# Kernel optimization log

Hardware: AMD Instinct MI355X
Metric: run time of the kernel (lower is better)

Reference implementation:

```python
import jax, jax.numpy as jnp
import numpy as np

# Module hyperparameters (init_kwargs)
TOP_K = 0.15          # fraction of pixels kept per row when step_percent=1
IGNORE_INDEX = 255

B, K, N, H, W = 8, 3, 8, 384, 384


def setup_inputs() -> dict:
    key = jax.random.key(0)
    k1, k2 = jax.random.split(key)
    # log-probabilities over K classes (nll_loss expects log-probs)
    logits = jax.random.normal(k1, (B, K, N, H, W), dtype=jnp.float32)
    inp = jax.nn.log_softmax(logits, axis=1)
    target = jax.random.randint(k2, (B, N, H, W), 0, K, dtype=jnp.int32)
    return {"input": inp, "target": target, "step_percent": 1}


def reference(input, target, step_percent):
    b, k, n, h, w = input.shape
    P = h * w
    x = input.reshape(b * n, k, P)           # (BN, K, P)
    t = target.reshape(b * n, P)             # (BN, P)

    # per-pixel NLL with ignore_index (ignored pixels contribute 0)
    mask = t != IGNORE_INDEX
    t_safe = jnp.where(mask, t, 0)
    nll = -jnp.take_along_axis(x, t_safe[:, None, :], axis=1)[:, 0, :]  # (BN, P)
    nll = jnp.where(mask, nll, jnp.zeros((), nll.dtype))

    # static k: step_percent is a Python scalar in the original forward
    sp = min(float(step_percent), 1.0)
    n_top_k = int(sp * TOP_K * P + (1.0 - sp) * P)

    top_k_loss, _ = jax.lax.top_k(nll, n_top_k)  # (BN, n_top_k)
    return jnp.mean(top_k_loss)
```

## Files before the change

kernel.cpp:

```cpp
#include <hip/hip_runtime.h>

#define BN    64
#define KCLS  3
#define PPIX  147456
#define NB1   4096
#define NB3   128
#define BPR   36
#define PX_BLK 4096
#define F4_BLK 1024
#define CAP   8192

static const size_t OFF_NLL  = 0;
static const size_t OFF_CAND = OFF_NLL + (size_t)BN * PPIX * 4;
static const size_t OFF_C1   = OFF_CAND + (size_t)BN * CAP * 4;
static const size_t OFF_CCNT = OFF_C1 + (size_t)BN * NB1 * 4;
static const size_t OFF_SS   = OFF_CCNT + 256;
static const size_t OFF_ACC  = OFF_SS + 512;
static const size_t ZERO_END = OFF_ACC + 8;

__device__ __forceinline__ unsigned topk_count(const int* sp_ptr) {
    double sp = (double)sp_ptr[0];
    if (sp > 1.0) sp = 1.0;
    return (unsigned)(sp * 0.15 * (double)PPIX + (1.0 - sp) * (double)PPIX);
}

__device__ __forceinline__ float sel_nll(int t, float a, float b, float c) {
    float lp = (t == 0) ? a : ((t == 1) ? b : ((t == 2) ? c : 0.0f));
    return fmaxf(-lp, 0.0f);
}

__global__ __launch_bounds__(256) void k_hist1(
    const float* __restrict__ in, const int* __restrict__ tgt,
    float* __restrict__ nll, unsigned* __restrict__ cnt1)
{
    __shared__ unsigned lc[NB1];
    const int tid = threadIdx.x;
    for (int i = tid; i < NB1; i += 256) lc[i] = 0u;
    __syncthreads();

    const int row   = blockIdx.x / BPR;
    const int chunk = blockIdx.x % BPR;
    const float4* p0 = (const float4*)(in + (size_t)row * KCLS * PPIX);
    const float4* p1 = p0 + PPIX / 4;
    const float4* p2 = p1 + PPIX / 4;
    const int4*   t4 = (const int4*)(tgt + (size_t)row * PPIX);
    float4*       n4 = (float4*)(nll + (size_t)row * PPIX);
    const int base = chunk * F4_BLK;

    #pragma unroll
    for (int j = 0; j < 4; ++j) {
        const int idx = base + j * 256 + tid;
        const int4   t = t4[idx];
        const float4 a = p0[idx];
        const float4 b = p1[idx];
        const float4 c = p2[idx];
        float4 v;
        v.x = sel_nll(t.x, a.x, b.x, c.x);
        v.y = sel_nll(t.y, a.y, b.y, c.y);
        v.z = sel_nll(t.z, a.z, b.z, c.z);
        v.w = sel_nll(t.w, a.w, b.w, c.w);
        n4[idx] = v;
        atomicAdd(&lc[__float_as_uint(v.x) >> 19], 1u);
        atomicAdd(&lc[__float_as_uint(v.y) >> 19], 1u);
        atomicAdd(&lc[__float_as_uint(v.z) >> 19], 1u);
        atomicAdd(&lc[__float_as_uint(v.w) >> 19], 1u);
    }
    __syncthreads();

    unsigned* gc = cnt1 + (size_t)row * NB1;
    for (int i = tid; i < NB1; i += 256) {
        const unsigned cc = lc[i];
        if (cc) atomicAdd(&gc[i], cc);
    }
}

__global__ __launch_bounds__(256) void k_scan(
    const unsigned* __restrict__ cnt, const int* __restrict__ sp_ptr,
    int* __restrict__ st_b, int* __restrict__ st_r)
{
    const int row = blockIdx.x, tid = threadIdx.x;
    __shared__ unsigned csum[256];
    const unsigned* c = cnt + (size_t)row * NB1;

    unsigned cl[16]; unsigned cacc = 0;
    const int base = tid * 16;
    #pragma unroll
    for (int i = 0; i < 16; ++i) {
        cl[i] = c[NB1 - 1 - (base + i)];
        cacc += cl[i];
    }
    csum[tid] = cacc;
    __syncthreads();
    for (int off = 1; off < 256; off <<= 1) {
        unsigned t2 = (tid >= off) ? csum[tid - off] : 0u;
        __syncthreads();
        csum[tid] += t2;
        __syncthreads();
    }
    const unsigned k = topk_count(sp_ptr);
    unsigned cum = tid ? csum[tid - 1] : 0u;
    #pragma unroll
    for (int i = 0; i < 16; ++i) {
        const unsigned cb = cl[i];
        if (cum < k && cum + cb >= k) {
            st_b[row] = NB1 - 1 - (base + i);
            st_r[row] = (int)(k - cum);
        }
        cum += cb;
    }
}

__global__ __launch_bounds__(256) void k_compact(
    const float* __restrict__ nll, const int* __restrict__ st_b1,
    float* __restrict__ cand, int* __restrict__ ccnt, double* __restrict__ st_S)
{
    __shared__ float  stage[PX_BLK];
    __shared__ double dred[256];
    __shared__ int lcnt, gbase;
    const int tid = threadIdx.x;
    if (tid == 0) lcnt = 0;
    __syncthreads();

    const int row   = blockIdx.x / BPR;
    const int chunk = blockIdx.x % BPR;
    const unsigned b1 = (unsigned)st_b1[row];
    const unsigned lo = b1 << 19;
    const unsigned hi = (b1 + 1u) << 19;
    const float4* n4 = (const float4*)(nll + (size_t)row * PPIX);
    const int base = chunk * F4_BLK;

    double acc = 0.0;
    #pragma unroll
    for (int j = 0; j < 4; ++j) {
        const float4 f = n4[base + j * 256 + tid];
        const float vv[4] = {f.x, f.y, f.z, f.w};
        #pragma unroll
        for (int q = 0; q < 4; ++q) {
            const unsigned u = __float_as_uint(vv[q]);
            if (u >= hi) {
                acc += (double)vv[q];
            } else if (u >= lo) {
                const int s = atomicAdd(&lcnt, 1);
                stage[s] = vv[q];
            }
        }
    }
    dred[tid] = acc;
    __syncthreads();
    for (int s = 128; s > 0; s >>= 1) {
        if (tid < s) dred[tid] += dred[tid + s];
        __syncthreads();
    }
    if (tid == 0) {
        atomicAdd(&st_S[row], dred[0]);
        gbase = atomicAdd(&ccnt[row], lcnt);
    }
    __syncthreads();
    const int n = lcnt, gb = gbase;
    float* cr = cand + (size_t)row * CAP;
    for (int i = tid; i < n; i += 256) {
        const int pos = gb + i;
        if (pos < CAP) cr[pos] = stage[i];
    }
}

__global__ __launch_bounds__(256) void k_resolve(
    const float* __restrict__ cand, const int* __restrict__ ccnt,
    const int* __restrict__ st_b1, const int* __restrict__ st_r1,
    const double* __restrict__ st_S, double* __restrict__ accum)
{
    __shared__ unsigned lc[NB1];
    __shared__ float    ls[NB1];
    __shared__ unsigned csum[256];
    __shared__ double   ssum[256];
    __shared__ int sb2, sr2;
    __shared__ double sS2;

    const int row = blockIdx.x, tid = threadIdx.x;
    int n = ccnt[row]; if (n > CAP) n = CAP;
    const float* cv = cand + (size_t)row * CAP;

    for (int i = tid; i < NB1; i += 256) { lc[i] = 0u; ls[i] = 0.0f; }
    __syncthreads();
    for (int i = tid; i < n; i += 256) {
        const float v = cv[i];
        const unsigned key = (__float_as_uint(v) >> 7) & 0xFFFu;
        atomicAdd(&lc[key], 1u);
        atomicAdd(&ls[key], v);
    }
    __syncthreads();

    unsigned cl[16]; float slv[16];
    unsigned cacc = 0; double sacc = 0.0;
    const int base = tid * 16;
    #pragma unroll
    for (int i = 0; i < 16; ++i) {
        const int bin = NB1 - 1 - (base + i);
        cl[i]  = lc[bin];
        slv[i] = ls[bin];
        cacc += cl[i];
        sacc += (double)slv[i];
    }
    csum[tid] = cacc; ssum[tid] = sacc;
    __syncthreads();
    for (int off = 1; off < 256; off <<= 1) {
        unsigned cv2 = 0; double sv = 0.0;
        if (tid >= off) { cv2 = csum[tid - off]; sv = ssum[tid - off]; }
        __syncthreads();
        csum[tid] += cv2; ssum[tid] += sv;
        __syncthreads();
    }
    const unsigned k = (unsigned)st_r1[row];
    unsigned cum = tid ? csum[tid - 1] : 0u;
    double   sS  = tid ? ssum[tid - 1] : 0.0;
    #pragma unroll
    for (int i = 0; i < 16; ++i) {
        const unsigned cb = cl[i];
        if (cum < k && cum + cb >= k) {
            sb2 = NB1 - 1 - (base + i);
            sr2 = (int)(k - cum);
            sS2 = sS;
        }
        cum += cb;
        sS  += (double)slv[i];
    }
    __syncthreads();

    const unsigned pref = ((unsigned)st_b1[row] << 12) | (unsigned)sb2;
    if (tid < NB3) { lc[tid] = 0u; ls[tid] = 0.0f; }
    __syncthreads();
    for (int i = tid; i < n; i += 256) {
        const float v = cv[i];
        const unsigned bits = __float_as_uint(v);
        if ((bits >> 7) == pref) {
            atomicAdd(&lc[bits & 0x7Fu], 1u);
            atomicAdd(&ls[bits & 0x7Fu], v);
        }
    }
    __syncthreads();
    if (tid == 0) {
        const unsigned k3 = (unsigned)sr2;
        unsigned cum3 = 0, r3 = 0; int b3 = 0; double S3 = 0.0;
        for (int bin = NB3 - 1; bin >= 0; --bin) {
            const unsigned cb = lc[bin];
            if (cum3 < k3 && cum3 + cb >= k3) { b3 = bin; r3 = k3 - cum3; break; }
            cum3 += cb;
            S3   += (double)ls[bin];
        }
        const float tval = __uint_as_float((pref << 7) | (unsigned)b3);
        const double total = st_S[row] + sS2 + S3 + (double)r3 * (double)tval;
        atomicAdd(accum, total);
    }
}

__global__ void k_out(const double* __restrict__ accum, const int* __restrict__ sp_ptr,
                      float* __restrict__ out)
{
    if (threadIdx.x == 0 && blockIdx.x == 0) {
        const unsigned k = topk_count(sp_ptr);
        out[0] = (float)(accum[0] / ((double)BN * (double)k));
    }
}

extern "C" void kernel_launch(void* const* d_in, const int* in_sizes, int n_in,
                              void* d_out, int out_size, void* d_ws, size_t ws_size,
                              hipStream_t stream)
{
    const float* in  = (const float*)d_in[0];
    const int*   tgt = (const int*)d_in[1];
    const int*   sp  = (const int*)d_in[2];

    char* ws = (char*)d_ws;
    float*    nll   = (float*)(ws + OFF_NLL);
    float*    cand  = (float*)(ws + OFF_CAND);
    unsigned* cnt1  = (unsigned*)(ws + OFF_C1);
    int*      ccnt  = (int*)(ws + OFF_CCNT);
    double*   st_S  = (double*)(ws + OFF_SS);
    double*   accum = (double*)(ws + OFF_ACC);
    int*      st_b1 = (int*)(ws + OFF_CCNT + 64 * 4);
    st_b1 = (int*)(ws + ZERO_END);
    int*  st_r1 = (int*)(ws + ZERO_END + 256);

    hipMemsetAsync(ws + OFF_C1, 0, ZERO_END - OFF_C1, stream);

    const int blocks = BN * BPR;
    k_hist1  <<<blocks, 256, 0, stream>>>(in, tgt, nll, cnt1);
    k_scan   <<<BN, 256, 0, stream>>>(cnt1, sp, st_b1, st_r1);
    k_compact<<<blocks, 256, 0, stream>>>(nll, st_b1, cand, ccnt, st_S);
    k_resolve<<<BN, 256, 0, stream>>>(cand, ccnt, st_b1, st_r1, st_S, accum);
    k_out    <<<1, 64, 0, stream>>>(accum, sp, (float*)d_out);
}
```

Baseline: 253.2 us.

## Fuse top-k radix-select pipeline into one cooperative kernel with register-resident NLL

Replaces the five-kernel histogram/scan/compact/resolve/output chain with a single cooperative kernel of 1024 blocks that uses grid-wide syncs between phases. Each thread keeps its per-pixel NLL values in registers across the first grid sync, so the full NLL buffer is never written to or read back from global memory. The scan is recomputed redundantly in every block and the final division happens through a ticket counter. This removes launch gaps and a large global round trip, at the cost of grid-sync overhead and a co-residency requirement of four blocks per CU. If the cooperative launch fails, it falls back to the old multi-kernel path.

```diff
diff --git a/kernel.cpp b/kernel.cpp
--- a/kernel.cpp
+++ b/kernel.cpp
@@ -1,14 +1,24 @@
 #include <hip/hip_runtime.h>
+#include <hip/hip_cooperative_groups.h>
+
+namespace cg = cooperative_groups;
 
 #define BN    64
 #define KCLS  3
 #define PPIX  147456
 #define NB1   4096
 #define NB3   128
-#define BPR   36
+#define CAP   8192
+
+#define NBLK      1024
+#define CPR       16
+#define F4PB      2304
+#define VPT       9
+#define STAGE_CAP 2048
+
+#define BPR    36
+#define F4_BLK 1024
 #define PX_BLK 4096
-#define F4_BLK 1024
-#define CAP   8192
 
 static const size_t OFF_NLL  = 0;
 static const size_t OFF_CAND = OFF_NLL + (size_t)BN * PPIX * 4;
@@ -16,7 +26,10 @@
 static const size_t OFF_CCNT = OFF_C1 + (size_t)BN * NB1 * 4;
 static const size_t OFF_SS   = OFF_CCNT + 256;
 static const size_t OFF_ACC  = OFF_SS + 512;
-static const size_t ZERO_END = OFF_ACC + 8;
+static const size_t OFF_DONE = OFF_ACC + 8;
+static const size_t ZERO_END = OFF_DONE + 8;
+static const size_t OFF_B1   = ZERO_END;
+static const size_t OFF_R1   = ZERO_END + 256;
 
 __device__ __forceinline__ unsigned topk_count(const int* sp_ptr) {
     double sp = (double)sp_ptr[0];
@@ -27,6 +40,246 @@
 __device__ __forceinline__ float sel_nll(int t, float a, float b, float c) {
     float lp = (t == 0) ? a : ((t == 1) ? b : ((t == 2) ? c : 0.0f));
     return fmaxf(-lp, 0.0f);
+}
+
+__device__ __forceinline__ unsigned ld_au32(const unsigned* p) {
+    return __hip_atomic_load(p, __ATOMIC_RELAXED, __HIP_MEMORY_SCOPE_AGENT);
+}
+__device__ __forceinline__ int ld_ai32(const int* p) {
+    return __hip_atomic_load(p, __ATOMIC_RELAXED, __HIP_MEMORY_SCOPE_AGENT);
+}
+__device__ __forceinline__ float ld_af32(const float* p) {
+    return __hip_atomic_load(p, __ATOMIC_RELAXED, __HIP_MEMORY_SCOPE_AGENT);
+}
+__device__ __forceinline__ double ld_af64(const double* p) {
+    return __hip_atomic_load(p, __ATOMIC_RELAXED, __HIP_MEMORY_SCOPE_AGENT);
+}
+
+struct SMemA { unsigned lc[NB1]; };
+struct SMemC { unsigned csum[256]; float stage[STAGE_CAP]; double dred[256]; };
+struct SMemD { unsigned lc[NB1]; float ls[NB1]; unsigned csum[256]; double ssum[256]; };
+union  SMemU { SMemA a; SMemC c; SMemD d; };
+
+__global__ __launch_bounds__(256, 4) void k_fused(
+    const float* __restrict__ in, const int* __restrict__ tgt,
+    const int* __restrict__ sp, unsigned* __restrict__ ghist,
+    float* __restrict__ cand, int* __restrict__ ccnt,
+    double* __restrict__ st_S, double* __restrict__ accum,
+    unsigned* __restrict__ done, float* __restrict__ out)
+{
+    __shared__ SMemU sm;
+    __shared__ int s_b1, s_r1, s_lcnt, s_gbase;
+    __shared__ int s_b2, s_r2;
+    __shared__ double s_S2;
+    cg::grid_group grid = cg::this_grid();
+
+    const int tid   = threadIdx.x;
+    const int bid   = blockIdx.x;
+    const int row   = bid >> 4;
+    const int chunk = bid & (CPR - 1);
+
+    for (int i = tid; i < NB1; i += 256) sm.a.lc[i] = 0u;
+    __syncthreads();
+
+    const float4* p0 = (const float4*)(in + (size_t)row * KCLS * PPIX);
+    const float4* p1 = p0 + PPIX / 4;
+    const float4* p2 = p1 + PPIX / 4;
+    const int4*   t4 = (const int4*)(tgt + (size_t)row * PPIX);
+    const int base = chunk * F4PB;
+
+    float4 v[VPT];
+    #pragma unroll
+    for (int j = 0; j < VPT; ++j) {
+        const int idx = base + j * 256 + tid;
+        const int4   t = t4[idx];
+        const float4 a = p0[idx];
+        const float4 b = p1[idx];
+        const float4 c = p2[idx];
+        float4 w;
+        w.x = sel_nll(t.x, a.x, b.x, c.x);
+        w.y = sel_nll(t.y, a.y, b.y, c.y);
+        w.z = sel_nll(t.z, a.z, b.z, c.z);
+        w.w = sel_nll(t.w, a.w, b.w, c.w);
+        v[j] = w;
+        atomicAdd(&sm.a.lc[__float_as_uint(w.x) >> 19], 1u);
+        atomicAdd(&sm.a.lc[__float_as_uint(w.y) >> 19], 1u);
+        atomicAdd(&sm.a.lc[__float_as_uint(w.z) >> 19], 1u);
+        atomicAdd(&sm.a.lc[__float_as_uint(w.w) >> 19], 1u);
+    }
+    __syncthreads();
+    {
+        unsigned* gh = ghist + (size_t)row * NB1;
+        for (int i = tid; i < NB1; i += 256) {
+            const unsigned cc = sm.a.lc[i];
+            if (cc) atomicAdd(&gh[i], cc);
+        }
+    }
+    grid.sync();
+
+    const unsigned* ghr = ghist + (size_t)row * NB1;
+    unsigned cl[16]; unsigned cacc = 0u;
+    const int cbase = tid * 16;
+    #pragma unroll
+    for (int i = 0; i < 16; ++i) {
+        cl[i] = ld_au32(&ghr[NB1 - 1 - (cbase + i)]);
+        cacc += cl[i];
+    }
+    sm.c.csum[tid] = cacc;
+    __syncthreads();
+    for (int off = 1; off < 256; off <<= 1) {
+        unsigned t2 = (tid >= off) ? sm.c.csum[tid - off] : 0u;
+        __syncthreads();
+        sm.c.csum[tid] += t2;
+        __syncthreads();
+    }
+    const unsigned k = topk_count(sp);
+    {
+        unsigned cum = tid ? sm.c.csum[tid - 1] : 0u;
+        #pragma unroll
+        for (int i = 0; i < 16; ++i) {
+            const unsigned cb = cl[i];
+            if (cum < k && cum + cb >= k) {
+                s_b1 = NB1 - 1 - (cbase + i);
+                s_r1 = (int)(k - cum);
+            }
+            cum += cb;
+        }
+    }
+    if (tid == 0) s_lcnt = 0;
+    __syncthreads();
+
+    const unsigned b1 = (unsigned)s_b1;
+    const unsigned lo = b1 << 19;
+    const unsigned hi = (b1 + 1u) << 19;
+    int*   ccr = &ccnt[row];
+    float* cr  = cand + (size_t)row * CAP;
+
+    double acc = 0.0;
+    #pragma unroll
+    for (int j = 0; j < VPT; ++j) {
+        const float vv[4] = {v[j].x, v[j].y, v[j].z, v[j].w};
+        #pragma unroll
+        for (int q = 0; q < 4; ++q) {
+            const unsigned u = __float_as_uint(vv[q]);
+            if (u >= hi) {
+                acc += (double)vv[q];
+            } else if (u >= lo) {
+                const int s = atomicAdd(&s_lcnt, 1);
+                if (s < STAGE_CAP) {
+                    sm.c.stage[s] = vv[q];
+                } else {
+                    const int gp = atomicAdd(ccr, 1);
+                    if (gp < CAP) cr[gp] = vv[q];
+                }
+            }
+        }
+    }
+    sm.c.dred[tid] = acc;
+    __syncthreads();
+    for (int s = 128; s > 0; s >>= 1) {
+        if (tid < s) sm.c.dred[tid] += sm.c.dred[tid + s];
+        __syncthreads();
+    }
+    if (tid == 0) {
+        atomicAdd(&st_S[row], sm.c.dred[0]);
+        int nst = s_lcnt; if (nst > STAGE_CAP) nst = STAGE_CAP;
+        s_gbase = atomicAdd(ccr, nst);
+    }
+    __syncthreads();
+    {
+        int nst = s_lcnt; if (nst > STAGE_CAP) nst = STAGE_CAP;
+        const int gb = s_gbase;
+        for (int i = tid; i < nst; i += 256) {
+            const int pos = gb + i;
+            if (pos < CAP) cr[pos] = sm.c.stage[i];
+        }
+    }
+    __threadfence();
+    grid.sync();
+
+    if (chunk != 0) return;
+
+    int n = ld_ai32(ccr); if (n > CAP) n = CAP;
+
+    for (int i = tid; i < NB1; i += 256) { sm.d.lc[i] = 0u; sm.d.ls[i] = 0.0f; }
+    __syncthreads();
+    for (int i = tid; i < n; i += 256) {
+        const float vv2 = ld_af32(&cr[i]);
+        const unsigned key = (__float_as_uint(vv2) >> 7) & 0xFFFu;
+        atomicAdd(&sm.d.lc[key], 1u);
+        atomicAdd(&sm.d.ls[key], vv2);
+    }
+    __syncthreads();
+
+    {
+        unsigned cl2[16]; float slv[16];
+        unsigned cacc2 = 0; double sacc = 0.0;
+        #pragma unroll
+        for (int i = 0; i < 16; ++i) {
+            const int bin = NB1 - 1 - (cbase + i);
+            cl2[i] = sm.d.lc[bin];
+            slv[i] = sm.d.ls[bin];
+            cacc2 += cl2[i];
+            sacc  += (double)slv[i];
+        }
+        sm.d.csum[tid] = cacc2; sm.d.ssum[tid] = sacc;
+        __syncthreads();
+        for (int off = 1; off < 256; off <<= 1) {
+            unsigned cv2 = 0; double sv = 0.0;
+            if (tid >= off) { cv2 = sm.d.csum[tid - off]; sv = sm.d.ssum[tid - off]; }
+            __syncthreads();
+            sm.d.csum[tid] += cv2; sm.d.ssum[tid] += sv;
+            __syncthreads();
+        }
+        const unsigned k2 = (unsigned)s_r1;
+        unsigned cum = tid ? sm.d.csum[tid - 1] : 0u;
+        double   sS  = tid ? sm.d.ssum[tid - 1] : 0.0;
+        #pragma unroll
+        for (int i = 0; i < 16; ++i) {
+            const unsigned cb = cl2[i];
+            if (cum < k2 && cum + cb >= k2) {
+                s_b2 = NB1 - 1 - (cbase + i);
+                s_r2 = (int)(k2 - cum);
+                s_S2 = sS;
+            }
+            cum += cb;
+            sS  += (double)slv[i];
+        }
+    }
+    __syncthreads();
+
+    const unsigned pref = ((unsigned)s_b1 << 12) | (unsigned)s_b2;
+    if (tid < NB3) { sm.d.lc[tid] = 0u; sm.d.ls[tid] = 0.0f; }
+    __syncthreads();
+    for (int i = tid; i < n; i += 256) {
+        const float vv2 = ld_af32(&cr[i]);
+        const unsigned bits = __float_as_uint(vv2);
+        if ((bits >> 7) == pref) {
+            atomicAdd(&sm.d.lc[bits & 0x7Fu], 1u);
+            atomicAdd(&sm.d.ls[bits & 0x7Fu], vv2);
+        }
+    }
+    __syncthreads();
+    if (tid == 0) {
+        const unsigned k3 = (unsigned)s_r2;
+        unsigned cum3 = 0, r3 = 0; int b3 = 0; double S3 = 0.0;
+        for (int bin = NB3 - 1; bin >= 0; --bin) {
+            const unsigned cb = sm.d.lc[bin];
+            if (cum3 < k3 && cum3 + cb >= k3) { b3 = bin; r3 = k3 - cum3; break; }
+            cum3 += cb;
+            S3   += (double)sm.d.ls[bin];
+        }
+        const float tval = __uint_as_float((pref << 7) | (unsigned)b3);
+        const double total = ld_af64(&st_S[row]) + s_S2 + S3 + (double)r3 * (double)tval;
+        atomicAdd(accum, total);
+        __threadfence();
+        const unsigned ticket = atomicAdd(done, 1u);
+        if (ticket == BN - 1) {
+            __threadfence();
+            const double a2 = ld_af64(accum);
+            out[0] = (float)(a2 / ((double)BN * (double)topk_count(sp)));
+        }
+    }
 }
 
 __global__ __launch_bounds__(256) void k_hist1(
@@ -266,6 +519,7 @@
                               void* d_out, int out_size, void* d_ws, size_t ws_size,
                               hipStream_t stream)
 {
+    (void)in_sizes; (void)n_in; (void)out_size; (void)ws_size;
     const float* in  = (const float*)d_in[0];
     const int*   tgt = (const int*)d_in[1];
     const int*   sp  = (const int*)d_in[2];
@@ -273,20 +527,30 @@
     char* ws = (char*)d_ws;
     float*    nll   = (float*)(ws + OFF_NLL);
     float*    cand  = (float*)(ws + OFF_CAND);
-    unsigned* cnt1  = (unsigned*)(ws + OFF_C1);
+    unsigned* ghist = (unsigned*)(ws + OFF_C1);
     int*      ccnt  = (int*)(ws + OFF_CCNT);
     double*   st_S  = (double*)(ws + OFF_SS);
     double*   accum = (double*)(ws + OFF_ACC);
-    int*      st_b1 = (int*)(ws + OFF_CCNT + 64 * 4);
-    st_b1 = (int*)(ws + ZERO_END);
-    int*  st_r1 = (int*)(ws + ZERO_END + 256);
+    unsigned* done  = (unsigned*)(ws + OFF_DONE);
+    int*      st_b1 = (int*)(ws + OFF_B1);
+    int*      st_r1 = (int*)(ws + OFF_R1);
+    float*    outp  = (float*)d_out;
 
     hipMemsetAsync(ws + OFF_C1, 0, ZERO_END - OFF_C1, stream);
 
-    const int blocks = BN * BPR;
-    k_hist1  <<<blocks, 256, 0, stream>>>(in, tgt, nll, cnt1);
-    k_scan   <<<BN, 256, 0, stream>>>(cnt1, sp, st_b1, st_r1);
-    k_compact<<<blocks, 256, 0, stream>>>(nll, st_b1, cand, ccnt, st_S);
-    k_resolve<<<BN, 256, 0, stream>>>(cand, ccnt, st_b1, st_r1, st_S, accum);
-    k_out    <<<1, 64, 0, stream>>>(accum, sp, (float*)d_out);
-}
+    void* kargs[] = {
+        (void*)&in, (void*)&tgt, (void*)&sp, (void*)&ghist, (void*)&cand,
+        (void*)&ccnt, (void*)&st_S, (void*)&accum, (void*)&done, (void*)&outp
+    };
+    hipError_t err = hipLaunchCooperativeKernel(
+        (const void*)k_fused, dim3(NBLK), dim3(256), kargs, 0, stream);
+
+    if (err != hipSuccess) {
+        const int blocks = BN * BPR;
+        k_hist1  <<<blocks, 256, 0, stream>>>(in, tgt, nll, ghist);
+        k_scan   <<<BN, 256, 0, stream>>>(ghist, sp, st_b1, st_r1);
+        k_compact<<<blocks, 256, 0, stream>>>(nll, st_b1, cand, ccnt, st_S);
+        k_resolve<<<BN, 256, 0, stream>>>(cand, ccnt, st_b1, st_r1, st_S, accum);
+        k_out    <<<1, 64, 0, stream>>>(accum, sp, (float*)d_out);
+    }
+}
```

Result: slower. 494.6 us (+95.3%).

## Fuse scan, compact and resolve into one per-row select kernel

Applied to the files above, without the earlier changes.

Replaces the scan, compact, resolve and output kernels with a single 1024-thread block per row. Each block finds the threshold bucket, scans the row's NLL values, stages candidates in shared memory, and refines the threshold with two more radix passes. The last block to finish writes the output, tracked with a ticket counter. This removes kernel launches and the global candidate buffer round trip, but runs only 64 blocks for the full read of the NLL buffer, which may leave much of the GPU idle.

```diff
diff --git a/kernel.cpp b/kernel.cpp
--- a/kernel.cpp
+++ b/kernel.cpp
@@ -4,19 +4,19 @@
 #define KCLS  3
 #define PPIX  147456
 #define NB1   4096
-#define NB3   128
-#define BPR   36
-#define PX_BLK 4096
+
+#define BPR    36
 #define F4_BLK 1024
-#define CAP   8192
+
+#define RS_THREADS 1024
+#define RS_F4      (PPIX / 4 / RS_THREADS)
+#define CAPS       8192
 
 static const size_t OFF_NLL  = 0;
-static const size_t OFF_CAND = OFF_NLL + (size_t)BN * PPIX * 4;
-static const size_t OFF_C1   = OFF_CAND + (size_t)BN * CAP * 4;
-static const size_t OFF_CCNT = OFF_C1 + (size_t)BN * NB1 * 4;
-static const size_t OFF_SS   = OFF_CCNT + 256;
-static const size_t OFF_ACC  = OFF_SS + 512;
-static const size_t ZERO_END = OFF_ACC + 8;
+static const size_t OFF_GH   = (size_t)BN * PPIX * 4;
+static const size_t OFF_ACC  = OFF_GH + (size_t)BN * NB1 * 4;
+static const size_t OFF_DONE = OFF_ACC + 8;
+static const size_t ZERO_END = OFF_DONE + 8;
 
 __device__ __forceinline__ unsigned topk_count(const int* sp_ptr) {
     double sp = (double)sp_ptr[0];
@@ -74,65 +74,62 @@
     }
 }
 
-__global__ __launch_bounds__(256) void k_scan(
-    const unsigned* __restrict__ cnt, const int* __restrict__ sp_ptr,
-    int* __restrict__ st_b, int* __restrict__ st_r)
+__global__ __launch_bounds__(RS_THREADS, 1) void k_rowselect(
+    const float* __restrict__ nll, const unsigned* __restrict__ ghist,
+    const int* __restrict__ sp, double* __restrict__ accum,
+    unsigned* __restrict__ done, float* __restrict__ out)
 {
-    const int row = blockIdx.x, tid = threadIdx.x;
-    __shared__ unsigned csum[256];
-    const unsigned* c = cnt + (size_t)row * NB1;
-
-    unsigned cl[16]; unsigned cacc = 0;
-    const int base = tid * 16;
+    __shared__ float    stage[CAPS];
+    __shared__ double   dd[RS_THREADS];
+    __shared__ unsigned cs[RS_THREADS];
+    __shared__ unsigned lc2[1024];
+    __shared__ float    ls2[1024];
+    __shared__ int s_b1, s_r1, s_lcnt, s_b2, s_r2;
+    __shared__ double s_S0, s_S2;
+
+    const int row = blockIdx.x;
+    const int tid = threadIdx.x;
+
+    const unsigned* ghr = ghist + (size_t)row * NB1;
+    unsigned cl[4]; unsigned cacc = 0u;
     #pragma unroll
-    for (int i = 0; i < 16; ++i) {
-        cl[i] = c[NB1 - 1 - (base + i)];
+    for (int i = 0; i < 4; ++i) {
+        cl[i] = ghr[NB1 - 1 - (tid * 4 + i)];
         cacc += cl[i];
     }
-    csum[tid] = cacc;
-    __syncthreads();
-    for (int off = 1; off < 256; off <<= 1) {
-        unsigned t2 = (tid >= off) ? csum[tid - off] : 0u;
-        __syncthreads();
-        csum[tid] += t2;
-        __syncthreads();
-    }
-    const unsigned k = topk_count(sp_ptr);
-    unsigned cum = tid ? csum[tid - 1] : 0u;
-    #pragma unroll
-    for (int i = 0; i < 16; ++i) {
-        const unsigned cb = cl[i];
-        if (cum < k && cum + cb >= k) {
-            st_b[row] = NB1 - 1 - (base + i);
-            st_r[row] = (int)(k - cum);
-        }
-        cum += cb;
-    }
-}
-
-__global__ __launch_bounds__(256) void k_compact(
-    const float* __restrict__ nll, const int* __restrict__ st_b1,
-    float* __restrict__ cand, int* __restrict__ ccnt, double* __restrict__ st_S)
-{
-    __shared__ float  stage[PX_BLK];
-    __shared__ double dred[256];
-    __shared__ int lcnt, gbase;
-    const int tid = threadIdx.x;
-    if (tid == 0) lcnt = 0;
-    __syncthreads();
-
-    const int row   = blockIdx.x / BPR;
-    const int chunk = blockIdx.x % BPR;
-    const unsigned b1 = (unsigned)st_b1[row];
+    cs[tid] = cacc;
+    __syncthreads();
+    for (int off = 1; off < RS_THREADS; off <<= 1) {
+        unsigned t2 = (tid >= off) ? cs[tid - off] : 0u;
+        __syncthreads();
+        cs[tid] += t2;
+        __syncthreads();
+    }
+    const unsigned k = topk_count(sp);
+    {
+        unsigned cum = tid ? cs[tid - 1] : 0u;
+        #pragma unroll
+        for (int i = 0; i < 4; ++i) {
+            const unsigned cb = cl[i];
+            if (cum < k && cum + cb >= k) {
+                s_b1 = NB1 - 1 - (tid * 4 + i);
+                s_r1 = (int)(k - cum);
+            }
+            cum += cb;
+        }
+    }
+    if (tid == 0) s_lcnt = 0;
+    __syncthreads();
+
+    const unsigned b1 = (unsigned)s_b1;
     const unsigned lo = b1 << 19;
     const unsigned hi = (b1 + 1u) << 19;
     const float4* n4 = (const float4*)(nll + (size_t)row * PPIX);
-    const int base = chunk * F4_BLK;
 
     double acc = 0.0;
     #pragma unroll
-    for (int j = 0; j < 4; ++j) {
-        const float4 f = n4[base + j * 256 + tid];
+    for (int j = 0; j < RS_F4; ++j) {
+        const float4 f = n4[j * RS_THREADS + tid];
         const float vv[4] = {f.x, f.y, f.z, f.w};
         #pragma unroll
         for (int q = 0; q < 4; ++q) {
@@ -140,125 +137,95 @@
             if (u >= hi) {
                 acc += (double)vv[q];
             } else if (u >= lo) {
-                const int s = atomicAdd(&lcnt, 1);
-                stage[s] = vv[q];
+                const int s = atomicAdd(&s_lcnt, 1);
+                if (s < CAPS) stage[s] = vv[q];
             }
         }
     }
-    dred[tid] = acc;
-    __syncthreads();
-    for (int s = 128; s > 0; s >>= 1) {
-        if (tid < s) dred[tid] += dred[tid + s];
-        __syncthreads();
-    }
-    if (tid == 0) {
-        atomicAdd(&st_S[row], dred[0]);
-        gbase = atomicAdd(&ccnt[row], lcnt);
-    }
-    __syncthreads();
-    const int n = lcnt, gb = gbase;
-    float* cr = cand + (size_t)row * CAP;
-    for (int i = tid; i < n; i += 256) {
-        const int pos = gb + i;
-        if (pos < CAP) cr[pos] = stage[i];
-    }
-}
-
-__global__ __launch_bounds__(256) void k_resolve(
-    const float* __restrict__ cand, const int* __restrict__ ccnt,
-    const int* __restrict__ st_b1, const int* __restrict__ st_r1,
-    const double* __restrict__ st_S, double* __restrict__ accum)
-{
-    __shared__ unsigned lc[NB1];
-    __shared__ float    ls[NB1];
-    __shared__ unsigned csum[256];
-    __shared__ double   ssum[256];
-    __shared__ int sb2, sr2;
-    __shared__ double sS2;
-
-    const int row = blockIdx.x, tid = threadIdx.x;
-    int n = ccnt[row]; if (n > CAP) n = CAP;
-    const float* cv = cand + (size_t)row * CAP;
-
-    for (int i = tid; i < NB1; i += 256) { lc[i] = 0u; ls[i] = 0.0f; }
-    __syncthreads();
-    for (int i = tid; i < n; i += 256) {
-        const float v = cv[i];
-        const unsigned key = (__float_as_uint(v) >> 7) & 0xFFFu;
-        atomicAdd(&lc[key], 1u);
-        atomicAdd(&ls[key], v);
-    }
-    __syncthreads();
-
-    unsigned cl[16]; float slv[16];
-    unsigned cacc = 0; double sacc = 0.0;
-    const int base = tid * 16;
-    #pragma unroll
-    for (int i = 0; i < 16; ++i) {
-        const int bin = NB1 - 1 - (base + i);
-        cl[i]  = lc[bin];
-        slv[i] = ls[bin];
-        cacc += cl[i];
-        sacc += (double)slv[i];
-    }
-    csum[tid] = cacc; ssum[tid] = sacc;
-    __syncthreads();
-    for (int off = 1; off < 256; off <<= 1) {
-        unsigned cv2 = 0; double sv = 0.0;
-        if (tid >= off) { cv2 = csum[tid - off]; sv = ssum[tid - off]; }
-        __syncthreads();
-        csum[tid] += cv2; ssum[tid] += sv;
-        __syncthreads();
-    }
-    const unsigned k = (unsigned)st_r1[row];
-    unsigned cum = tid ? csum[tid - 1] : 0u;
-    double   sS  = tid ? ssum[tid - 1] : 0.0;
-    #pragma unroll
-    for (int i = 0; i < 16; ++i) {
-        const unsigned cb = cl[i];
-        if (cum < k && cum + cb >= k) {
-            sb2 = NB1 - 1 - (base + i);
-            sr2 = (int)(k - cum);
-            sS2 = sS;
-        }
-        cum += cb;
-        sS  += (double)slv[i];
-    }
-    __syncthreads();
-
-    const unsigned pref = ((unsigned)st_b1[row] << 12) | (unsigned)sb2;
-    if (tid < NB3) { lc[tid] = 0u; ls[tid] = 0.0f; }
-    __syncthreads();
-    for (int i = tid; i < n; i += 256) {
-        const float v = cv[i];
+    dd[tid] = acc;
+    __syncthreads();
+    for (int s = RS_THREADS / 2; s > 0; s >>= 1) {
+        if (tid < s) dd[tid] += dd[tid + s];
+        __syncthreads();
+    }
+    if (tid == 0) s_S0 = dd[0];
+    int n = s_lcnt; if (n > CAPS) n = CAPS;
+
+    lc2[tid] = 0u; ls2[tid] = 0.0f;
+    __syncthreads();
+    for (int i = tid; i < n; i += RS_THREADS) {
+        const float v = stage[i];
+        const unsigned key = (__float_as_uint(v) >> 9) & 0x3FFu;
+        atomicAdd(&lc2[key], 1u);
+        atomicAdd(&ls2[key], v);
+    }
+    __syncthreads();
+
+    {
+        const unsigned c2 = lc2[1023 - tid];
+        const float    f2 = ls2[1023 - tid];
+        cs[tid] = c2; dd[tid] = (double)f2;
+        __syncthreads();
+        for (int off = 1; off < RS_THREADS; off <<= 1) {
+            unsigned tc = 0u; double td = 0.0;
+            if (tid >= off) { tc = cs[tid - off]; td = dd[tid - off]; }
+            __syncthreads();
+            cs[tid] += tc; dd[tid] += td;
+            __syncthreads();
+        }
+        const unsigned k2 = (unsigned)s_r1;
+        const unsigned cum = tid ? cs[tid - 1] : 0u;
+        const double   sS  = tid ? dd[tid - 1] : 0.0;
+        if (cum < k2 && cum + c2 >= k2) {
+            s_b2 = 1023 - tid;
+            s_r2 = (int)(k2 - cum);
+            s_S2 = sS;
+        }
+    }
+    __syncthreads();
+
+    const unsigned b2 = (unsigned)s_b2;
+    if (tid < 512) { lc2[tid] = 0u; ls2[tid] = 0.0f; }
+    __syncthreads();
+    for (int i = tid; i < n; i += RS_THREADS) {
+        const float v = stage[i];
         const unsigned bits = __float_as_uint(v);
-        if ((bits >> 7) == pref) {
-            atomicAdd(&lc[bits & 0x7Fu], 1u);
-            atomicAdd(&ls[bits & 0x7Fu], v);
-        }
-    }
-    __syncthreads();
-    if (tid == 0) {
-        const unsigned k3 = (unsigned)sr2;
-        unsigned cum3 = 0, r3 = 0; int b3 = 0; double S3 = 0.0;
-        for (int bin = NB3 - 1; bin >= 0; --bin) {
-            const unsigned cb = lc[bin];
-            if (cum3 < k3 && cum3 + cb >= k3) { b3 = bin; r3 = k3 - cum3; break; }
-            cum3 += cb;
-            S3   += (double)ls[bin];
-        }
-        const float tval = __uint_as_float((pref << 7) | (unsigned)b3);
-        const double total = st_S[row] + sS2 + S3 + (double)r3 * (double)tval;
-        atomicAdd(accum, total);
-    }
-}
-
-__global__ void k_out(const double* __restrict__ accum, const int* __restrict__ sp_ptr,
-                      float* __restrict__ out)
-{
-    if (threadIdx.x == 0 && blockIdx.x == 0) {
-        const unsigned k = topk_count(sp_ptr);
-        out[0] = (float)(accum[0] / ((double)BN * (double)k));
+        if (((bits >> 9) & 0x3FFu) == b2) {
+            atomicAdd(&lc2[bits & 0x1FFu], 1u);
+            atomicAdd(&ls2[bits & 0x1FFu], v);
+        }
+    }
+    __syncthreads();
+    {
+        const unsigned c3 = (tid < 512) ? lc2[511 - tid] : 0u;
+        const float    f3 = (tid < 512) ? ls2[511 - tid] : 0.0f;
+        cs[tid] = c3; dd[tid] = (double)f3;
+        __syncthreads();
+        for (int off = 1; off < RS_THREADS; off <<= 1) {
+            unsigned tc = 0u; double td = 0.0;
+            if (tid >= off) { tc = cs[tid - off]; td = dd[tid - off]; }
+            __syncthreads();
+            cs[tid] += tc; dd[tid] += td;
+            __syncthreads();
+        }
+        const unsigned k3 = (unsigned)s_r2;
+        const unsigned cum = tid ? cs[tid - 1] : 0u;
+        const double   S3  = tid ? dd[tid - 1] : 0.0;
+        if (cum < k3 && cum + c3 >= k3) {
+            const int      bin3 = 511 - tid;
+            const unsigned r3   = k3 - cum;
+            const float tval = __uint_as_float((b1 << 19) | (b2 << 9) | (unsigned)bin3);
+            const double total = s_S0 + s_S2 + S3 + (double)r3 * (double)tval;
+            atomicAdd(accum, total);
+            __threadfence();
+            const unsigned ticket =
+                __hip_atomic_fetch_add(done, 1u, __ATOMIC_ACQ_REL, __HIP_MEMORY_SCOPE_AGENT);
+            if (ticket == BN - 1) {
+                const double a2 =
+                    __hip_atomic_load(accum, __ATOMIC_RELAXED, __HIP_MEMORY_SCOPE_AGENT);
+                out[0] = (float)(a2 / ((double)BN * (double)topk_count(sp)));
+            }
+        }
     }
 }
 
@@ -266,27 +233,20 @@
                               void* d_out, int out_size, void* d_ws, size_t ws_size,
                               hipStream_t stream)
 {
+    (void)in_sizes; (void)n_in; (void)out_size; (void)ws_size;
     const float* in  = (const float*)d_in[0];
     const int*   tgt = (const int*)d_in[1];
     const int*   sp  = (const int*)d_in[2];
 
     char* ws = (char*)d_ws;
     float*    nll   = (float*)(ws + OFF_NLL);
-    float*    cand  = (float*)(ws + OFF_CAND);
-    unsigned* cnt1  = (unsigned*)(ws + OFF_C1);
-    int*      ccnt  = (int*)(ws + OFF_CCNT);
-    double*   st_S  = (double*)(ws + OFF_SS);
+    unsigned* ghist = (unsigned*)(ws + OFF_GH);
     double*   accum = (double*)(ws + OFF_ACC);
-    int*      st_b1 = (int*)(ws + OFF_CCNT + 64 * 4);
-    st_b1 = (int*)(ws + ZERO_END);
-    int*  st_r1 = (int*)(ws + ZERO_END + 256);
-
-    hipMemsetAsync(ws + OFF_C1, 0, ZERO_END - OFF_C1, stream);
-
-    const int blocks = BN * BPR;
-    k_hist1  <<<blocks, 256, 0, stream>>>(in, tgt, nll, cnt1);
-    k_scan   <<<BN, 256, 0, stream>>>(cnt1, sp, st_b1, st_r1);
-    k_compact<<<blocks, 256, 0, stream>>>(nll, st_b1, cand, ccnt, st_S);
-    k_resolve<<<BN, 256, 0, stream>>>(cand, ccnt, st_b1, st_r1, st_S, accum);
-    k_out    <<<1, 64, 0, stream>>>(accum, sp, (float*)d_out);
-}
+    unsigned* done  = (unsigned*)(ws + OFF_DONE);
+
+    hipMemsetAsync(ws + OFF_GH, 0, ZERO_END - OFF_GH, stream);
+
+    k_hist1    <<<BN * BPR, 256,        0, stream>>>(in, tgt, nll, ghist);
+    k_rowselect<<<BN,       RS_THREADS, 0, stream>>>(nll, ghist, sp, accum, done,
+                                                     (float*)d_out);
+}
```

Result: faster. 244.0 us (-3.6%).
